# Kernel tuning notes

Hardware: AMD Instinct MI355X
Metric: run time of the kernel (lower is better)

Reference implementation:

```python
import jax, jax.numpy as jnp
import numpy as np

D_IN = 1024
D_OUT = 1024
NUM_HEADS = 16
HEAD_DIM = D_OUT // NUM_HEADS


def setup_inputs() -> dict:
    key = jax.random.key(0)
    ks = jax.random.split(key, 6)
    s = 0.02
    return {
        "x": jax.random.normal(ks[0], (4, 2048, D_IN), dtype=jnp.float32),
        "Wq": jax.random.normal(ks[1], (D_IN, D_OUT), dtype=jnp.float32) * s,
        "Wk": jax.random.normal(ks[2], (D_IN, D_OUT), dtype=jnp.float32) * s,
        "Wv": jax.random.normal(ks[3], (D_IN, D_OUT), dtype=jnp.float32) * s,
        "Wo": jax.random.normal(ks[4], (D_OUT, D_OUT), dtype=jnp.float32) * s,
        "bo": jax.random.normal(ks[5], (D_OUT,), dtype=jnp.float32) * s,
    }


def reference(x, Wq, Wk, Wv, Wo, bo):
    B, T, _ = x.shape
    H, Dh = NUM_HEADS, HEAD_DIM
    # projections -> [B, H, T, Dh]
    q = (x @ Wq).reshape(B, T, H, Dh).transpose(0, 2, 1, 3)
    k = (x @ Wk).reshape(B, T, H, Dh).transpose(0, 2, 1, 3)
    v = (x @ Wv).reshape(B, T, H, Dh).transpose(0, 2, 1, 3)
    # scores [B, H, T, T]
    scores = jnp.einsum('bhqd,bhkd->bhqk', q, k)
    causal = jnp.triu(jnp.ones((T, T), dtype=bool), k=1)
    scores = jnp.where(causal, -jnp.inf, scores)
    attn = jax.nn.softmax(scores / jnp.sqrt(jnp.float32(Dh)), axis=-1)
    # dropout=0.0 -> identity
    ctx = jnp.einsum('bhqk,bhkd->bhqd', attn, v)
    ctx = ctx.transpose(0, 2, 1, 3).reshape(B, T, H * Dh)
    return ctx @ Wo + bo
```

## Files before the change

### kernel.cpp

```cpp
#include <hip/hip_runtime.h>
#include <hip/hip_bf16.h>
#include <stdint.h>

#define TSEQ 2048
#define DMODEL 1024

typedef __attribute__((ext_vector_type(8))) short bf16x8;
typedef __attribute__((ext_vector_type(4))) float f32x4;
typedef __attribute__((ext_vector_type(16))) float f32x16;

union Frag { bf16x8 v; uint4 q; };

__device__ __forceinline__ uint16_t f2bfu(float f) {
  uint32_t u = __builtin_bit_cast(uint32_t, f);
  u += 0x7fffu + ((u >> 16) & 1u);
  return (uint16_t)(u >> 16);
}

__device__ __forceinline__ uint32_t pk2bf(float a, float b) {
  return ((uint32_t)f2bfu(b) << 16) | f2bfu(a);
}

__device__ __forceinline__ float fexp2(float x) {
#if __has_builtin(__builtin_amdgcn_exp2f)
  return __builtin_amdgcn_exp2f(x);
#else
  return exp2f(x);
#endif
}

__device__ __forceinline__ void gload_lds16(const void* g, void* l) {
  __builtin_amdgcn_global_load_lds(
      (const __attribute__((address_space(1))) void*)g,
      (__attribute__((address_space(3))) void*)l, 16, 0, 0);
}


__global__ __launch_bounds__(256) void cvt_x_kernel(const float* __restrict__ x,
                                                    uint16_t* __restrict__ xb, int n4) {
  int i = blockIdx.x * 256 + threadIdx.x;
  if (i >= n4) return;
  float4 v = ((const float4*)x)[i];
  ushort4 o;
  o.x = f2bfu(v.x); o.y = f2bfu(v.y); o.z = f2bfu(v.z); o.w = f2bfu(v.w);
  ((ushort4*)xb)[i] = o;
}

__global__ __launch_bounds__(256) void cvt_w_kernel(const float* __restrict__ Wq,
    const float* __restrict__ Wk, const float* __restrict__ Wv, const float* __restrict__ Wo,
    uint16_t* __restrict__ Wqkvt, uint16_t* __restrict__ Wot) {
  const float* src = (blockIdx.z == 0) ? Wq : (blockIdx.z == 1) ? Wk
                   : (blockIdx.z == 2) ? Wv : Wo;
  uint16_t* dst = (blockIdx.z < 3) ? (Wqkvt + (size_t)blockIdx.z * DMODEL * DMODEL) : Wot;
  const float wscale = (blockIdx.z == 0) ? 0.125f * 1.4426950408889634f : 1.0f;
  __shared__ float tile[32][33];
  const int x0 = blockIdx.x * 32, y0 = blockIdx.y * 32;
  for (int ii = 0; ii < 4; ii++) {
    int i = threadIdx.y + ii * 8;
    tile[i][threadIdx.x] = src[(size_t)(y0 + i) * DMODEL + x0 + threadIdx.x];
  }
  __syncthreads();
  for (int ii = 0; ii < 4; ii++) {
    int i = threadIdx.y + ii * 8;
    dst[(size_t)(x0 + i) * DMODEL + y0 + threadIdx.x] = f2bfu(tile[threadIdx.x][i] * wscale);
  }
}


__device__ __forceinline__ void g8_stage(const char* Ab, const char* Bb, int kb,
                                         char* ldsA, char* ldsB, int tid) {
#pragma unroll
  for (int r = 0; r < 4; ++r) {
    const int u = tid + r * 512;
    const int row = u >> 3;
    const int sc = ((u & 7) * 16) ^ ((row & 7) << 4);
    gload_lds16(Ab + (size_t)row * 2048 + kb + sc, ldsA + u * 16);
  }
#pragma unroll
  for (int r = 0; r < 2; ++r) {
    const int u = tid + r * 512;
    const int row = u >> 3;
    const int sc = ((u & 7) * 16) ^ ((row & 7) << 4);
    gload_lds16(Bb + (size_t)row * 2048 + kb + sc, ldsB + u * 16);
  }
}

__device__ __forceinline__ void gemm256x128_core(const char* Ab, const char* Bb,
                                                 char* lds,
                                                 f32x4 (&acc)[4][4]) {
  const int tid = threadIdx.x;
  const int lane = tid & 63;
  const int w = tid >> 6;
  const int lr = lane & 15, lg = lane >> 4;
  const int wmb = (w >> 1) * 64;
  const int wnb = (w & 1) * 64;
  char* const A0 = lds;
  char* const A1 = lds + 32768;
  char* const B0 = lds + 65536;
  char* const B1 = lds + 81920;

#pragma unroll
  for (int i = 0; i < 4; i++)
#pragma unroll
    for (int j = 0; j < 4; j++) acc[i][j] = (f32x4){0.f, 0.f, 0.f, 0.f};

  g8_stage(Ab, Bb, 0, A0, B0, tid);
  for (int t = 0; t < 16; ++t) {
    if (t + 1 < 16) {
      char* nA = (t & 1) ? A0 : A1;
      char* nB = (t & 1) ? B0 : B1;
      g8_stage(Ab, Bb, (t + 1) * 128, nA, nB, tid);
      asm volatile("s_waitcnt vmcnt(6)" ::: "memory");
    } else {
      asm volatile("s_waitcnt vmcnt(0)" ::: "memory");
    }
    __builtin_amdgcn_s_barrier();
    __builtin_amdgcn_sched_barrier(0);
    const char* At = (t & 1) ? A1 : A0;
    const char* Bt = (t & 1) ? B1 : B0;

    Frag bf0[4], bf1[4];
#pragma unroll
    for (int ni = 0; ni < 4; ni++) {
      const int row = wnb + ni * 16 + lr;
      const int swz = (row & 7) << 4;
      bf0[ni].q = *(const uint4*)(Bt + row * 128 + ((lg * 16) ^ swz));
      bf1[ni].q = *(const uint4*)(Bt + row * 128 + ((64 + lg * 16) ^ swz));
    }
#pragma unroll
    for (int mi = 0; mi < 4; mi++) {
      const int row = wmb + mi * 16 + lr;
      const int swz = (row & 7) << 4;
      Frag a0, a1;
      a0.q = *(const uint4*)(At + row * 128 + ((lg * 16) ^ swz));
      a1.q = *(const uint4*)(At + row * 128 + ((64 + lg * 16) ^ swz));
      __builtin_amdgcn_s_setprio(1);
#pragma unroll
      for (int ni = 0; ni < 4; ni++) {
        acc[mi][ni] = __builtin_amdgcn_mfma_f32_16x16x32_bf16(a0.v, bf0[ni].v,
                                                              acc[mi][ni], 0, 0, 0);
        acc[mi][ni] = __builtin_amdgcn_mfma_f32_16x16x32_bf16(a1.v, bf1[ni].v,
                                                              acc[mi][ni], 0, 0, 0);
      }
      __builtin_amdgcn_s_setprio(0);
      __builtin_amdgcn_s_barrier();
    }
  }
}


__global__ __launch_bounds__(512, 2) void gemm_qkv_kernel(const uint16_t* __restrict__ Xb,
    const uint16_t* __restrict__ Wt, uint16_t* __restrict__ Qo,
    uint16_t* __restrict__ Ko, uint16_t* __restrict__ Vt) {
  __shared__ __align__(16) char lds[98304];
  const int m0 = (blockIdx.x & 31) * 256;
  const int n0 = (blockIdx.x >> 5) * 128;
  f32x4 acc[4][4];
  gemm256x128_core((const char*)Xb + (size_t)m0 * 2048, (const char*)Wt + (size_t)n0 * 2048,
                   lds, acc);

  const int tid = threadIdx.x, w = tid >> 6, lane = tid & 63;
  const int lr = lane & 15, lg = lane >> 4;
  const int wmb = (w >> 1) * 64, wnb = (w & 1) * 64;

  if (n0 >= 2048) {
    char* vr = lds + (w & 1) * 33792;
#pragma unroll
    for (int mi = 0; mi < 4; mi++)
#pragma unroll
      for (int ni = 0; ni < 4; ni++) {
        const int d = ni * 16 + lr;
        const int tl = wmb + mi * 16 + 4 * lg;
        uint2 pr;
        pr.x = pk2bf(acc[mi][ni][0], acc[mi][ni][1]);
        pr.y = pk2bf(acc[mi][ni][2], acc[mi][ni][3]);
        *(uint2*)(vr + d * 528 + tl * 2) = pr;
      }
    __syncthreads();
    const int bb = m0 >> 11, t0 = m0 & 2047;
    const int h0 = (n0 - 2048) >> 6;
#pragma unroll
    for (int j = 0; j < 8; j++) {
      const int linear = (tid + j * 512) * 16;
      const int rg = linear >> 15;
      const int rem = linear & 32767;
      const int d = rem >> 9;
      const int toff = rem & 511;
      const uint4 val = *(const uint4*)(lds + rg * 33792 + d * 528 + toff);
      const int bh = bb * 16 + h0 + rg;
      *(uint4*)((char*)Vt + ((size_t)(bh * 64 + d) * TSEQ + t0) * 2 + toff) = val;
    }
  } else {
#pragma unroll
    for (int mi = 0; mi < 4; mi++)
#pragma unroll
      for (int ni = 0; ni < 4; ni++) {
        const int col = n0 + wnb + ni * 16 + lr;
        const int p = col >> 10, c = col & 1023, h = c >> 6, d = c & 63;
#pragma unroll
        for (int r = 0; r < 4; r++) {
          const int row = m0 + wmb + mi * 16 + 4 * lg + r;
          const int bb = row >> 11, t = row & 2047;
          const int bh = bb * 16 + h;
          const uint16_t val = f2bfu(acc[mi][ni][r]);
          if (p == 0) Qo[((size_t)bh * TSEQ + t) * 64 + d] = val;
          else        Ko[((size_t)bh * TSEQ + t) * 64 + d] = val;
        }
      }
  }
}


__device__ __forceinline__ void stage_kv(const char* Kb, const char* Vb, int kv0,
                                         char* kdst, char* vdst, int tid) {
  const int w1024 = (tid >> 6) * 1024;
#pragma unroll
  for (int i = 0; i < 2; i++) {
    const int o = i * 4096 + tid * 16;
    const int row = o >> 7;
    const int scol = (o & 127) ^ ((row & 7) << 4);
    gload_lds16(Kb + (size_t)(kv0 + row) * 128 + scol, kdst + i * 4096 + w1024);
    gload_lds16(Vb + (size_t)row * 4096 + kv0 * 2 + scol, vdst + i * 4096 + w1024);
  }
}

__global__ __launch_bounds__(256, 3) void attn_kernel(const uint16_t* __restrict__ Qw,
    const uint16_t* __restrict__ Kw, const uint16_t* __restrict__ Vtw,
    uint16_t* __restrict__ Ctx) {
  const int bid = blockIdx.x;
  const int qt = 15 - (bid >> 6);
  const int bh = bid & 63;
  const int tid = threadIdx.x;
  const int w = tid >> 6, lane = tid & 63;
  const int lq = lane & 31;
  const int hi = lane >> 5;
  const int wq0 = qt * 128 + w * 32;

  const char* Qb = (const char*)Qw + (size_t)bh * TSEQ * 128;
  const char* Kb = (const char*)Kw + (size_t)bh * TSEQ * 128;
  const char* Vb = (const char*)Vtw + (size_t)bh * 64 * 4096;

  __shared__ __align__(16) char kbuf[2][8192];
  __shared__ __align__(16) char vbuf[2][8192];

  Frag qa[4];
#pragma unroll
  for (int kc = 0; kc < 4; kc++)
    qa[kc].q = *(const uint4*)(Qb + (size_t)(wq0 + lq) * 128 + kc * 32 + hi * 16);

  f32x16 o0 = 0.f, o1 = 0.f;
  float mrun = -1e30f, lrun = 0.f;

  const int nt = 2 * qt + 2;
  stage_kv(Kb, Vb, 0, kbuf[0], vbuf[0], tid);
  int cur = 0;
  for (int t = 0; t < nt; ++t) {
    const int kv0 = t * 64;
    if (t + 1 < nt) {
      stage_kv(Kb, Vb, kv0 + 64, kbuf[cur ^ 1], vbuf[cur ^ 1], tid);
      asm volatile("s_waitcnt vmcnt(4)" ::: "memory");
    } else {
      asm volatile("s_waitcnt vmcnt(0)" ::: "memory");
    }
    __builtin_amdgcn_s_barrier();
    __builtin_amdgcn_sched_barrier(0);

    if (kv0 <= wq0 + 31) {
      const char* Kt = kbuf[cur];
      const char* Vt = vbuf[cur];
      f32x16 s[2];
#pragma unroll
      for (int kvh = 0; kvh < 2; kvh++) {
        f32x16 acc = 0.f;
#pragma unroll
        for (int kc = 0; kc < 4; kc++) {
          const int row = kvh * 32 + lq;
          Frag kf;
          kf.q = *(const uint4*)(Kt + row * 128 + ((kc * 32 + hi * 16) ^ ((row & 7) << 4)));
          acc = __builtin_amdgcn_mfma_f32_32x32x16_bf16(kf.v, qa[kc].v, acc, 0, 0, 0);
        }
        s[kvh] = acc;
      }
      if (kv0 + 63 > wq0) {
        const int q_abs = wq0 + lq;
#pragma unroll
        for (int kvh = 0; kvh < 2; kvh++)
#pragma unroll
          for (int r = 0; r < 16; r++) {
            const int kv_abs = kv0 + kvh * 32 + (r & 3) + 8 * (r >> 2) + 4 * hi;
            if (kv_abs > q_abs) s[kvh][r] = -1e30f;
          }
      }
      float mt = s[0][0];
#pragma unroll
      for (int r = 1; r < 16; r++) mt = fmaxf(mt, s[0][r]);
#pragma unroll
      for (int r = 0; r < 16; r++) mt = fmaxf(mt, s[1][r]);
      mt = fmaxf(mt, __shfl_xor(mt, 32));
      const float mnew = fmaxf(mrun, mt);
      const float corr = fexp2(mrun - mnew);
      mrun = mnew;
#pragma unroll
      for (int kvh = 0; kvh < 2; kvh++)
#pragma unroll
        for (int r = 0; r < 16; r++) s[kvh][r] = fexp2(s[kvh][r] - mnew);
      float ps = 0.f;
#pragma unroll
      for (int kvh = 0; kvh < 2; kvh++)
#pragma unroll
        for (int r = 0; r < 16; r++) ps += s[kvh][r];
      ps += __shfl_xor(ps, 32);
      lrun = lrun * corr + ps;
      o0 *= corr;
      o1 *= corr;
      uint32_t pk[2][8];
#pragma unroll
      for (int kvh = 0; kvh < 2; kvh++)
#pragma unroll
        for (int j = 0; j < 8; j++)
          pk[kvh][j] = pk2bf(s[kvh][2 * j], s[kvh][2 * j + 1]);
#pragma unroll
      for (int c16 = 0; c16 < 4; c16++) {
        const int kvh = c16 >> 1, cl = c16 & 1;
        const uint32_t s0 = (uint32_t)__shfl_xor((int)pk[kvh][4 * cl + 0], 32);
        const uint32_t s1 = (uint32_t)__shfl_xor((int)pk[kvh][4 * cl + 1], 32);
        const uint32_t s2 = (uint32_t)__shfl_xor((int)pk[kvh][4 * cl + 2], 32);
        const uint32_t s3 = (uint32_t)__shfl_xor((int)pk[kvh][4 * cl + 3], 32);
        Frag pb;
        pb.q.x = hi ? s2 : pk[kvh][4 * cl + 0];
        pb.q.y = hi ? s3 : pk[kvh][4 * cl + 1];
        pb.q.z = hi ? pk[kvh][4 * cl + 2] : s0;
        pb.q.w = hi ? pk[kvh][4 * cl + 3] : s1;
#pragma unroll
        for (int dblk = 0; dblk < 2; dblk++) {
          const int row = dblk * 32 + lq;
          Frag vf;
          vf.q = *(const uint4*)(Vt + row * 128 + ((c16 * 32 + hi * 16) ^ ((row & 7) << 4)));
          if (dblk == 0)
            o0 = __builtin_amdgcn_mfma_f32_32x32x16_bf16(vf.v, pb.v, o0, 0, 0, 0);
          else
            o1 = __builtin_amdgcn_mfma_f32_32x32x16_bf16(vf.v, pb.v, o1, 0, 0, 0);
        }
      }
    }
    __builtin_amdgcn_s_barrier();
    cur ^= 1;
  }

  const int bb = bh >> 4, hh = bh & 15;
  const float inv = 1.0f / lrun;
  const int q_abs = wq0 + lq;
  uint16_t* crow = Ctx + ((size_t)bb * TSEQ + q_abs) * DMODEL + hh * 64;
#pragma unroll
  for (int dblk = 0; dblk < 2; dblk++)
#pragma unroll
    for (int g = 0; g < 4; g++) {
      const float a0 = (dblk ? o1[4 * g + 0] : o0[4 * g + 0]) * inv;
      const float a1 = (dblk ? o1[4 * g + 1] : o0[4 * g + 1]) * inv;
      const float a2 = (dblk ? o1[4 * g + 2] : o0[4 * g + 2]) * inv;
      const float a3 = (dblk ? o1[4 * g + 3] : o0[4 * g + 3]) * inv;
      uint2 st;
      st.x = pk2bf(a0, a1);
      st.y = pk2bf(a2, a3);
      *(uint2*)(crow + dblk * 32 + 8 * g + 4 * hi) = st;
    }
}


__global__ __launch_bounds__(512, 2) void gemm_out_kernel(const uint16_t* __restrict__ Cb,
    const uint16_t* __restrict__ Wot, const float* __restrict__ bo,
    float* __restrict__ out) {
  __shared__ __align__(16) char lds[98304];
  const int m0 = (blockIdx.x & 31) * 256;
  const int n0 = (blockIdx.x >> 5) * 128;
  f32x4 acc[4][4];
  gemm256x128_core((const char*)Cb + (size_t)m0 * 2048, (const char*)Wot + (size_t)n0 * 2048,
                   lds, acc);

  const int tid = threadIdx.x, w = tid >> 6, lane = tid & 63;
  const int lr = lane & 15, lg = lane >> 4;
  const int wmb = (w >> 1) * 64, wnb = (w & 1) * 64;
#pragma unroll
  for (int mi = 0; mi < 4; mi++)
#pragma unroll
    for (int ni = 0; ni < 4; ni++) {
      const int col = n0 + wnb + ni * 16 + lr;
      const float bias = bo[col];
#pragma unroll
      for (int r = 0; r < 4; r++) {
        const int row = m0 + wmb + mi * 16 + 4 * lg + r;
        out[(size_t)row * DMODEL + col] = acc[mi][ni][r] + bias;
      }
    }
}


extern "C" void kernel_launch(void* const* d_in, const int* in_sizes, int n_in,
                              void* d_out, int out_size, void* d_ws, size_t ws_size,
                              hipStream_t stream) {
  const float* x  = (const float*)d_in[0];
  const float* Wq = (const float*)d_in[1];
  const float* Wk = (const float*)d_in[2];
  const float* Wv = (const float*)d_in[3];
  const float* Wo = (const float*)d_in[4];
  const float* bo = (const float*)d_in[5];
  float* out = (float*)d_out;

  char* ws = (char*)d_ws;
  uint16_t* Xb    = (uint16_t*)(ws);
  uint16_t* Ctx   = (uint16_t*)(ws);
  uint16_t* Wqkvt = (uint16_t*)(ws + (16u << 20));
  uint16_t* Wot   = (uint16_t*)(ws + (22u << 20));
  uint16_t* Qw    = (uint16_t*)(ws + (24u << 20));
  uint16_t* Kw    = (uint16_t*)(ws + (40u << 20));
  uint16_t* Vtw   = (uint16_t*)(ws + (56u << 20));
  (void)ws_size; (void)in_sizes; (void)n_in; (void)out_size;

  cvt_x_kernel<<<8192, 256, 0, stream>>>(x, Xb, 2097152);
  cvt_w_kernel<<<dim3(32, 32, 4), dim3(32, 8), 0, stream>>>(Wq, Wk, Wv, Wo, Wqkvt, Wot);
  gemm_qkv_kernel<<<768, 512, 0, stream>>>(Xb, Wqkvt, Qw, Kw, Vtw);
  attn_kernel<<<1024, 256, 0, stream>>>(Qw, Kw, Vtw, Ctx);
  gemm_out_kernel<<<256, 512, 0, stream>>>(Ctx, Wot, bo, out);
}
```

Before: 184.9 us.

## Split GEMM tile prefetch into two phases and drop per-row-block barriers

The global-to-LDS prefetch for the next K-slice is split in two. Three of the four A loads are issued at the top of the iteration. The remaining A load and the B loads are issued in the middle of the MFMA work, after the first half of the row blocks. The wait count is reduced to match, and the per-mi barrier inside the compute loop becomes a single barrier at the end of each iteration. This spreads memory traffic across the compute phase and removes three barriers per K-step, in exchange for more complex vmcnt bookkeeping and higher register pressure from preloading two A fragments.

```diff
diff --git a/kernel.cpp b/kernel.cpp
--- a/kernel.cpp
+++ b/kernel.cpp
@@ -67,11 +67,20 @@
 }
 
 
-__device__ __forceinline__ void g8_stage(const char* Ab, const char* Bb, int kb,
-                                         char* ldsA, char* ldsB, int tid) {
-#pragma unroll
-  for (int r = 0; r < 4; ++r) {
+__device__ __forceinline__ void g8_stage_p1(const char* Ab, int kb, char* ldsA, int tid) {
+#pragma unroll
+  for (int r = 0; r < 3; ++r) {
     const int u = tid + r * 512;
+    const int row = u >> 3;
+    const int sc = ((u & 7) * 16) ^ ((row & 7) << 4);
+    gload_lds16(Ab + (size_t)row * 2048 + kb + sc, ldsA + u * 16);
+  }
+}
+
+__device__ __forceinline__ void g8_stage_p2(const char* Ab, const char* Bb, int kb,
+                                            char* ldsA, char* ldsB, int tid) {
+  {
+    const int u = tid + 3 * 512;
     const int row = u >> 3;
     const int sc = ((u & 7) * 16) ^ ((row & 7) << 4);
     gload_lds16(Ab + (size_t)row * 2048 + kb + sc, ldsA + u * 16);
@@ -104,20 +113,21 @@
 #pragma unroll
     for (int j = 0; j < 4; j++) acc[i][j] = (f32x4){0.f, 0.f, 0.f, 0.f};
 
-  g8_stage(Ab, Bb, 0, A0, B0, tid);
+  g8_stage_p1(Ab, 0, A0, tid);
+  g8_stage_p2(Ab, Bb, 0, A0, B0, tid);
   for (int t = 0; t < 16; ++t) {
+    const char* At = (t & 1) ? A1 : A0;
+    const char* Bt = (t & 1) ? B1 : B0;
+    char* nA = (t & 1) ? A0 : A1;
+    char* nB = (t & 1) ? B0 : B1;
     if (t + 1 < 16) {
-      char* nA = (t & 1) ? A0 : A1;
-      char* nB = (t & 1) ? B0 : B1;
-      g8_stage(Ab, Bb, (t + 1) * 128, nA, nB, tid);
-      asm volatile("s_waitcnt vmcnt(6)" ::: "memory");
+      g8_stage_p1(Ab, (t + 1) * 128, nA, tid);
+      asm volatile("s_waitcnt vmcnt(3)" ::: "memory");
     } else {
       asm volatile("s_waitcnt vmcnt(0)" ::: "memory");
     }
     __builtin_amdgcn_s_barrier();
     __builtin_amdgcn_sched_barrier(0);
-    const char* At = (t & 1) ? A1 : A0;
-    const char* Bt = (t & 1) ? B1 : B0;
 
     Frag bf0[4], bf1[4];
 #pragma unroll
@@ -127,24 +137,45 @@
       bf0[ni].q = *(const uint4*)(Bt + row * 128 + ((lg * 16) ^ swz));
       bf1[ni].q = *(const uint4*)(Bt + row * 128 + ((64 + lg * 16) ^ swz));
     }
-#pragma unroll
-    for (int mi = 0; mi < 4; mi++) {
+    Frag pa0[2], pa1[2];
+#pragma unroll
+    for (int mi = 0; mi < 2; mi++) {
       const int row = wmb + mi * 16 + lr;
       const int swz = (row & 7) << 4;
-      Frag a0, a1;
-      a0.q = *(const uint4*)(At + row * 128 + ((lg * 16) ^ swz));
-      a1.q = *(const uint4*)(At + row * 128 + ((64 + lg * 16) ^ swz));
+      pa0[mi].q = *(const uint4*)(At + row * 128 + ((lg * 16) ^ swz));
+      pa1[mi].q = *(const uint4*)(At + row * 128 + ((64 + lg * 16) ^ swz));
+    }
+    __builtin_amdgcn_s_setprio(1);
+#pragma unroll
+    for (int mi = 0; mi < 2; mi++)
+#pragma unroll
+      for (int ni = 0; ni < 4; ni++) {
+        acc[mi][ni] = __builtin_amdgcn_mfma_f32_16x16x32_bf16(pa0[mi].v, bf0[ni].v,
+                                                              acc[mi][ni], 0, 0, 0);
+        acc[mi][ni] = __builtin_amdgcn_mfma_f32_16x16x32_bf16(pa1[mi].v, bf1[ni].v,
+                                                              acc[mi][ni], 0, 0, 0);
+      }
+    __builtin_amdgcn_s_setprio(0);
+
+    if (t + 1 < 16) g8_stage_p2(Ab, Bb, (t + 1) * 128, nA, nB, tid);
+#pragma unroll
+    for (int mi = 2; mi < 4; mi++) {
+      const int row = wmb + mi * 16 + lr;
+      const int swz = (row & 7) << 4;
+      Frag qa0, qa1;
+      qa0.q = *(const uint4*)(At + row * 128 + ((lg * 16) ^ swz));
+      qa1.q = *(const uint4*)(At + row * 128 + ((64 + lg * 16) ^ swz));
       __builtin_amdgcn_s_setprio(1);
 #pragma unroll
       for (int ni = 0; ni < 4; ni++) {
-        acc[mi][ni] = __builtin_amdgcn_mfma_f32_16x16x32_bf16(a0.v, bf0[ni].v,
+        acc[mi][ni] = __builtin_amdgcn_mfma_f32_16x16x32_bf16(qa0.v, bf0[ni].v,
                                                               acc[mi][ni], 0, 0, 0);
-        acc[mi][ni] = __builtin_amdgcn_mfma_f32_16x16x32_bf16(a1.v, bf1[ni].v,
+        acc[mi][ni] = __builtin_amdgcn_mfma_f32_16x16x32_bf16(qa1.v, bf1[ni].v,
                                                               acc[mi][ni], 0, 0, 0);
       }
       __builtin_amdgcn_s_setprio(0);
-      __builtin_amdgcn_s_barrier();
-    }
+    }
+    __builtin_amdgcn_s_barrier();
   }
 }
 
```

Measured after the change: 185.4 us. No clear change (+0.3%).
